# Performance work log

Hardware: AMD Instinct MI355X
Metric: run time of the kernel (lower is better)

The kernel has to match this reference:

```python
import jax, jax.numpy as jnp
import numpy as np

N = 8192        # num nodes == input_dim (attn is [N,N], indexed by edge endpoints)
E = 262144      # num edges (nnz of sparse G), avg degree 32
OD = 64         # output_dim


def setup_inputs() -> dict:
    key = jax.random.key(0)
    k_x, k_r, k_c, k_v, k_a, k_w = jax.random.split(key, 6)
    x = jax.random.normal(k_x, (N, N), dtype=jnp.float32)
    row = jax.random.randint(k_r, (E,), 0, N)
    col = jax.random.randint(k_c, (E,), 0, N)
    values = jax.random.uniform(k_v, (E,), dtype=jnp.float32)
    attn = jax.random.uniform(k_a, (N, N), dtype=jnp.float32)  # init uniform(0,1) per reset_parameters
    stdv = 1.0 / np.sqrt(OD)
    weight = jax.random.uniform(k_w, (N, OD), dtype=jnp.float32, minval=-stdv, maxval=stdv)
    return {"x": x, "attn": attn, "weight": weight, "values": values, "row": row, "col": col}


def reference(x, attn, weight, values, row, col):
    # x = x @ W : [N, OD]
    y = x @ weight
    # sparse_dense_mul: scale each edge's value by attn[row, col] (irregular gather)
    ev = values * attn[row, col]                      # [E]
    # torch.sparse.mm(G, y): out[i] = sum_{e: row[e]==i} ev[e] * y[col[e]]
    out = jax.ops.segment_sum(ev[:, None] * y[col], row, num_segments=x.shape[0])
    return (out, jnp.linalg.norm(attn))
```

## Files before the change

### kernel.cpp

```cpp
#include <hip/hip_runtime.h>
#include <hip/hip_bf16.h>

#define N 8192
#define OD 64
#define E_EDGES 262144

#define BM 64
#define BK 64
#define KSPLIT 16
#define KS_PER_SPLIT (N / KSPLIT)
#define NTILES (KS_PER_SPLIT / BK)
#define SCAT_BLOCKS 8192
#define EDGE_ITERS (E_EDGES / (SCAT_BLOCKS * 4))

typedef __attribute__((ext_vector_type(8))) short bf16x8;
typedef __attribute__((ext_vector_type(4))) float f32x4;

__device__ __forceinline__ unsigned short f2bf(float f) {
    union { float f; unsigned u; } v; v.f = f;
    unsigned r = (v.u + 0x7fffu + ((v.u >> 16) & 1u)) >> 16;
    return (unsigned short)r;
}

__device__ __forceinline__ void gload16(const void* g, void* l) {
    __builtin_amdgcn_global_load_lds(
        (const __attribute__((address_space(1))) unsigned int*)g,
        (__attribute__((address_space(3))) unsigned int*)l, 16, 0, 0);
}

__global__ __launch_bounds__(256) void prep_kernel(const float* __restrict__ w,
                                                   unsigned short* __restrict__ wt,
                                                   float4* __restrict__ y4,
                                                   float4* __restrict__ out4) {
    const int bid = blockIdx.x, t = threadIdx.x;
    const int base = bid * 256 + t;
    float4 z{0.f, 0.f, 0.f, 0.f};
    #pragma unroll
    for (int u = 0; u < 4; ++u) y4[base + u * 32768] = z;
    #pragma unroll
    for (int u = 0; u < 4; ++u) out4[base + u * 32768] = z;

    __shared__ unsigned short lds[64][80];
    const int kb = bid * 64;
    #pragma unroll
    for (int p = 0; p < 4; ++p) {
        int idx = p * 1024 + t * 4;
        int r = idx >> 6, c = idx & 63;
        float4 v = *(const float4*)(&w[(size_t)(kb + r) * OD + c]);
        lds[c + 0][r] = f2bf(v.x);
        lds[c + 1][r] = f2bf(v.y);
        lds[c + 2][r] = f2bf(v.z);
        lds[c + 3][r] = f2bf(v.w);
    }
    __syncthreads();
    const int colx = t >> 2, j0 = (t & 3) * 16;
    #pragma unroll
    for (int u = 0; u < 2; ++u) {
        *(bf16x8*)(wt + (size_t)colx * N + kb + j0 + u * 8) =
            *(const bf16x8*)(&lds[colx][j0 + u * 8]);
    }
}

__global__ __launch_bounds__(256) void gemm_kernel(const float* __restrict__ x,
                                                   const unsigned short* __restrict__ wt,
                                                   float* __restrict__ y) {
    __shared__ float xs[2][BM * BK];
    __shared__ unsigned short bs[2][BM * BK];

    const int t = threadIdx.x;
    const int wv = t >> 6, lane = t & 63;
    const int lrow = lane & 15, g = lane >> 4;
    const int sw = lrow & 7;
    const int row0 = blockIdx.x * BM;
    const int k0 = blockIdx.y * KS_PER_SPLIT;

    const int xrow_b = t >> 4, xchunk = t & 15;
    const int brow_b = t >> 3, bchunk = t & 7;

    f32x4 acc[4] = {f32x4{0,0,0,0}, f32x4{0,0,0,0}, f32x4{0,0,0,0}, f32x4{0,0,0,0}};

    #define STAGE(buf, tile)                                                          \
        {                                                                             \
            const int kk = k0 + (tile) * BK;                                          \
            _Pragma("unroll")                                                         \
            for (int j = 0; j < 4; ++j) {                                             \
                int r = j * 16 + xrow_b;                                              \
                gload16(&x[(size_t)(row0 + r) * N + kk + ((xchunk ^ (r & 7)) << 2)],  \
                        &xs[buf][j * 1024 + t * 4]);                                  \
            }                                                                         \
            _Pragma("unroll")                                                         \
            for (int j = 0; j < 2; ++j) {                                             \
                int r = j * 32 + brow_b;                                              \
                gload16(&wt[(size_t)r * N + kk + ((bchunk ^ (r & 7)) << 3)],          \
                        &bs[buf][j * 2048 + t * 8]);                                  \
            }                                                                         \
        }

    STAGE(0, 0);
    asm volatile("s_waitcnt vmcnt(0)" ::: "memory");
    __syncthreads();

    int cur = 0;
    for (int tile = 0; tile < NTILES; ++tile) {
        if (tile + 1 < NTILES) STAGE(cur ^ 1, tile + 1);
        const int ar = wv * 16 + lrow;
        #pragma unroll
        for (int ks = 0; ks < 2; ++ks) {
            const int c0 = ks * 8 + g * 2;
            float4 lo = *(const float4*)&xs[cur][ar * 64 + ((c0 ^ sw) << 2)];
            float4 hi = *(const float4*)&xs[cur][ar * 64 + (((c0 + 1) ^ sw) << 2)];
            bf16x8 a;
            a[0] = f2bf(lo.x); a[1] = f2bf(lo.y); a[2] = f2bf(lo.z); a[3] = f2bf(lo.w);
            a[4] = f2bf(hi.x); a[5] = f2bf(hi.y); a[6] = f2bf(hi.z); a[7] = f2bf(hi.w);
            #pragma unroll
            for (int cf = 0; cf < 4; ++cf) {
                const int rb = cf * 16 + lrow;
                bf16x8 b = *(const bf16x8*)&bs[cur][rb * 64 + (((ks * 4 + g) ^ sw) << 3)];
                acc[cf] = __builtin_amdgcn_mfma_f32_16x16x32_bf16(a, b, acc[cf], 0, 0, 0);
            }
        }
        asm volatile("s_waitcnt vmcnt(0)" ::: "memory");
        __syncthreads();
        cur ^= 1;
    }

    float* yp = y + ((size_t)row0 + wv * 16 + g * 4) * OD;
    #pragma unroll
    for (int cf = 0; cf < 4; ++cf) {
        #pragma unroll
        for (int i = 0; i < 4; ++i)
            atomicAdd(&yp[i * OD + cf * 16 + lrow], acc[cf][i]);
    }
    #undef STAGE
}

__device__ __forceinline__ void do_scatter(const float* __restrict__ values,
                                           const float* __restrict__ attn,
                                           const int* __restrict__ row,
                                           const int* __restrict__ col,
                                           const float* __restrict__ y,
                                           float* __restrict__ out,
                                           int bid, int t) {
    const int lane = t & 63;
    const int w = t >> 6;
    int r8[EDGE_ITERS], c8[EDGE_ITERS];
    float v8[EDGE_ITERS], a8[EDGE_ITERS];
    #pragma unroll
    for (int i = 0; i < EDGE_ITERS; ++i) {
        int e = bid * 4 + w + i * (SCAT_BLOCKS * 4);
        r8[i] = row[e]; c8[i] = col[e]; v8[i] = values[e];
    }
    #pragma unroll
    for (int i = 0; i < EDGE_ITERS; ++i)
        a8[i] = attn[(size_t)r8[i] * N + c8[i]];
    #pragma unroll
    for (int i = 0; i < EDGE_ITERS; ++i) {
        float yv = y[c8[i] * OD + lane];
        atomicAdd(&out[r8[i] * OD + lane], v8[i] * a8[i] * yv);
    }
}

__device__ __forceinline__ float do_norm_part(const float* __restrict__ attn, int bid, int t) {
    const float4* a4 = (const float4*)attn;
    float s = 0.f;
    int i = bid * 256 + t;
    #pragma unroll
    for (int u = 0; u < 8; ++u) {
        float4 v = a4[i + u * (SCAT_BLOCKS * 256)];
        s += v.x * v.x + v.y * v.y + v.z * v.z + v.w * v.w;
    }
    return s;
}

__global__ __launch_bounds__(256) void scatter_norm_kernel(
        const float* __restrict__ values, const float* __restrict__ attn,
        const int* __restrict__ row, const int* __restrict__ col,
        const float* __restrict__ y, float* __restrict__ out,
        float* __restrict__ part) {
    const int bid = blockIdx.x, t = threadIdx.x;
    float s;
    if (bid & 1) {
        s = do_norm_part(attn, bid, t);
        do_scatter(values, attn, row, col, y, out, bid, t);
    } else {
        do_scatter(values, attn, row, col, y, out, bid, t);
        s = do_norm_part(attn, bid, t);
    }
    for (int off = 32; off > 0; off >>= 1) s += __shfl_down(s, off, 64);
    __shared__ float wpart[4];
    int wid = t >> 6;
    if ((t & 63) == 0) wpart[wid] = s;
    __syncthreads();
    if (t == 0) part[bid] = wpart[0] + wpart[1] + wpart[2] + wpart[3];
}

__global__ __launch_bounds__(256) void finalize_kernel(const float* __restrict__ part,
                                                       float* __restrict__ out_norm) {
    float s = 0.f;
    #pragma unroll
    for (int k = 0; k < SCAT_BLOCKS / 256; ++k) s += part[k * 256 + threadIdx.x];
    for (int off = 32; off > 0; off >>= 1) s += __shfl_down(s, off, 64);
    __shared__ float wp[4];
    int wid = threadIdx.x >> 6;
    if ((threadIdx.x & 63) == 0) wp[wid] = s;
    __syncthreads();
    if (threadIdx.x == 0) *out_norm = sqrtf(wp[0] + wp[1] + wp[2] + wp[3]);
}

extern "C" void kernel_launch(void* const* d_in, const int* in_sizes, int n_in,
                              void* d_out, int out_size, void* d_ws, size_t ws_size,
                              hipStream_t stream) {
    const float* x      = (const float*)d_in[0];
    const float* attn   = (const float*)d_in[1];
    const float* weight = (const float*)d_in[2];
    const float* values = (const float*)d_in[3];
    const int*   row    = (const int*)d_in[4];
    const int*   col    = (const int*)d_in[5];
    float* out = (float*)d_out;

    char* wsb = (char*)d_ws;
    float*          part = (float*)wsb;
    unsigned short* wt   = (unsigned short*)(wsb + (1u << 20));
    float*          y    = (float*)(wsb + (2u << 20));

    prep_kernel<<<128, 256, 0, stream>>>(weight, wt, (float4*)y, (float4*)out);
    gemm_kernel<<<dim3(N / BM, KSPLIT), 256, 0, stream>>>(x, wt, y);
    scatter_norm_kernel<<<SCAT_BLOCKS, 256, 0, stream>>>(values, attn, row, col, y, out, part);
    finalize_kernel<<<1, 256, 0, stream>>>(part, out + (size_t)N * OD);
}
```

Measured before the change: 164.7 us.

## Move attn norm reduction into GEMM tail and fold finalize into scatter

The streaming sum of squares over attn moves out of the scatter kernel and into the tail of each GEMM block, so each block reads a contiguous 32K-float slice. The separate finalize kernel is removed; one extra block in the scatter launch reduces the per-block partials and writes the norm. This cuts one kernel launch and leaves the scatter kernel purely gather/atomic-bound. The cost is that the GEMM kernel now carries a large extra sequential read, and the norm traffic no longer overlaps with the latency-bound scatter work.

```diff
diff --git a/kernel.cpp b/kernel.cpp
--- a/kernel.cpp
+++ b/kernel.cpp
@@ -10,6 +10,7 @@
 #define KSPLIT 16
 #define KS_PER_SPLIT (N / KSPLIT)
 #define NTILES (KS_PER_SPLIT / BK)
+#define GEMM_BLOCKS (N / BM * KSPLIT)
 #define SCAT_BLOCKS 8192
 #define EDGE_ITERS (E_EDGES / (SCAT_BLOCKS * 4))
 
@@ -61,9 +62,11 @@
     }
 }
 
-__global__ __launch_bounds__(256) void gemm_kernel(const float* __restrict__ x,
-                                                   const unsigned short* __restrict__ wt,
-                                                   float* __restrict__ y) {
+__global__ __launch_bounds__(256) void gemm_norm_kernel(const float* __restrict__ x,
+                                                        const unsigned short* __restrict__ wt,
+                                                        float* __restrict__ y,
+                                                        const float* __restrict__ attn,
+                                                        float* __restrict__ part) {
     __shared__ float xs[2][BM * BK];
     __shared__ unsigned short bs[2][BM * BK];
 
@@ -132,79 +135,63 @@
             atomicAdd(&yp[i * OD + cf * 16 + lrow], acc[cf][i]);
     }
     #undef STAGE
-}
-
-__device__ __forceinline__ void do_scatter(const float* __restrict__ values,
-                                           const float* __restrict__ attn,
-                                           const int* __restrict__ row,
-                                           const int* __restrict__ col,
-                                           const float* __restrict__ y,
-                                           float* __restrict__ out,
-                                           int bid, int t) {
-    const int lane = t & 63;
-    const int w = t >> 6;
-    int r8[EDGE_ITERS], c8[EDGE_ITERS];
-    float v8[EDGE_ITERS], a8[EDGE_ITERS];
-    #pragma unroll
-    for (int i = 0; i < EDGE_ITERS; ++i) {
-        int e = bid * 4 + w + i * (SCAT_BLOCKS * 4);
-        r8[i] = row[e]; c8[i] = col[e]; v8[i] = values[e];
-    }
-    #pragma unroll
-    for (int i = 0; i < EDGE_ITERS; ++i)
-        a8[i] = attn[(size_t)r8[i] * N + c8[i]];
-    #pragma unroll
-    for (int i = 0; i < EDGE_ITERS; ++i) {
-        float yv = y[c8[i] * OD + lane];
-        atomicAdd(&out[r8[i] * OD + lane], v8[i] * a8[i] * yv);
-    }
-}
-
-__device__ __forceinline__ float do_norm_part(const float* __restrict__ attn, int bid, int t) {
+
     const float4* a4 = (const float4*)attn;
+    const int fbid = blockIdx.y * (N / BM) + blockIdx.x;
+    const long nbase = (long)fbid * 8192;
     float s = 0.f;
-    int i = bid * 256 + t;
-    #pragma unroll
-    for (int u = 0; u < 8; ++u) {
-        float4 v = a4[i + u * (SCAT_BLOCKS * 256)];
+    #pragma unroll 8
+    for (int u = 0; u < 32; ++u) {
+        float4 v = a4[nbase + u * 256 + t];
         s += v.x * v.x + v.y * v.y + v.z * v.z + v.w * v.w;
-    }
-    return s;
-}
-
-__global__ __launch_bounds__(256) void scatter_norm_kernel(
-        const float* __restrict__ values, const float* __restrict__ attn,
-        const int* __restrict__ row, const int* __restrict__ col,
-        const float* __restrict__ y, float* __restrict__ out,
-        float* __restrict__ part) {
-    const int bid = blockIdx.x, t = threadIdx.x;
-    float s;
-    if (bid & 1) {
-        s = do_norm_part(attn, bid, t);
-        do_scatter(values, attn, row, col, y, out, bid, t);
-    } else {
-        do_scatter(values, attn, row, col, y, out, bid, t);
-        s = do_norm_part(attn, bid, t);
     }
     for (int off = 32; off > 0; off >>= 1) s += __shfl_down(s, off, 64);
     __shared__ float wpart[4];
     int wid = t >> 6;
     if ((t & 63) == 0) wpart[wid] = s;
     __syncthreads();
-    if (t == 0) part[bid] = wpart[0] + wpart[1] + wpart[2] + wpart[3];
-}
-
-__global__ __launch_bounds__(256) void finalize_kernel(const float* __restrict__ part,
-                                                       float* __restrict__ out_norm) {
-    float s = 0.f;
-    #pragma unroll
-    for (int k = 0; k < SCAT_BLOCKS / 256; ++k) s += part[k * 256 + threadIdx.x];
-    for (int off = 32; off > 0; off >>= 1) s += __shfl_down(s, off, 64);
-    __shared__ float wp[4];
-    int wid = threadIdx.x >> 6;
-    if ((threadIdx.x & 63) == 0) wp[wid] = s;
-    __syncthreads();
-    if (threadIdx.x == 0) *out_norm = sqrtf(wp[0] + wp[1] + wp[2] + wp[3]);
+    if (t == 0) part[fbid] = wpart[0] + wpart[1] + wpart[2] + wpart[3];
+}
+
+__global__ __launch_bounds__(256) void scatter_kernel(const float* __restrict__ values,
+                                                      const float* __restrict__ attn,
+                                                      const int* __restrict__ row,
+                                                      const int* __restrict__ col,
+                                                      const float* __restrict__ y,
+                                                      float* __restrict__ out,
+                                                      const float* __restrict__ part,
+                                                      float* __restrict__ out_norm) {
+    const int t = threadIdx.x;
+    if (blockIdx.x == SCAT_BLOCKS) {
+        float s = 0.f;
+        #pragma unroll
+        for (int k = 0; k < GEMM_BLOCKS / 256; ++k) s += part[k * 256 + t];
+        for (int off = 32; off > 0; off >>= 1) s += __shfl_down(s, off, 64);
+        __shared__ float wp[4];
+        int wid = t >> 6;
+        if ((t & 63) == 0) wp[wid] = s;
+        __syncthreads();
+        if (t == 0) *out_norm = sqrtf(wp[0] + wp[1] + wp[2] + wp[3]);
+        return;
+    }
+    const int bid = blockIdx.x;
+    const int lane = t & 63;
+    const int w = t >> 6;
+    int r8[EDGE_ITERS], c8[EDGE_ITERS];
+    float v8[EDGE_ITERS], a8[EDGE_ITERS];
+    #pragma unroll
+    for (int i = 0; i < EDGE_ITERS; ++i) {
+        int e = bid * 4 + w + i * (SCAT_BLOCKS * 4);
+        r8[i] = row[e]; c8[i] = col[e]; v8[i] = values[e];
+    }
+    #pragma unroll
+    for (int i = 0; i < EDGE_ITERS; ++i)
+        a8[i] = attn[(size_t)r8[i] * N + c8[i]];
+    #pragma unroll
+    for (int i = 0; i < EDGE_ITERS; ++i) {
+        float yv = y[c8[i] * OD + lane];
+        atomicAdd(&out[r8[i] * OD + lane], v8[i] * a8[i] * yv);
+    }
 }
 
 extern "C" void kernel_launch(void* const* d_in, const int* in_sizes, int n_in,
@@ -224,7 +211,7 @@
     float*          y    = (float*)(wsb + (2u << 20));
 
     prep_kernel<<<128, 256, 0, stream>>>(weight, wt, (float4*)y, (float4*)out);
-    gemm_kernel<<<dim3(N / BM, KSPLIT), 256, 0, stream>>>(x, wt, y);
-    scatter_norm_kernel<<<SCAT_BLOCKS, 256, 0, stream>>>(values, attn, row, col, y, out, part);
-    finalize_kernel<<<1, 256, 0, stream>>>(part, out + (size_t)N * OD);
-}
+    gemm_norm_kernel<<<dim3(N / BM, KSPLIT), 256, 0, stream>>>(x, wt, y, attn, part);
+    scatter_kernel<<<SCAT_BLOCKS + 1, 256, 0, stream>>>(values, attn, row, col, y, out,
+                                                        part, out + (size_t)N * OD);
+}
```

After: 183.9 us. 1.12x slower.
